# Performance work log

Measured on AMD Instinct MI355X. Metric: run time of the kernel, lower is better.

Reference implementation:

```python
import jax, jax.numpy as jnp
import numpy as np

INF = 1.0e7   # matches torch INF = 1.0 * 10000000.0
EOS_ID = 2
FIN_INIT = -1.0e9  # finite stand-in for torch's -inf init of fin_log_probs


def setup_inputs() -> dict:
    key = jax.random.key(0)
    k1, k2, k3, k4, k5, k6 = jax.random.split(key, 6)
    P, D, S, V = 32, 8, 2048, 128000
    # next-token probability distribution per (prompt, draft)
    logits = jax.random.normal(k1, (P * D, V), dtype=jnp.float32)
    probs = jax.nn.softmax(logits, axis=-1)
    alive_seq = jax.random.randint(k2, (P, D, S), 0, V, dtype=jnp.int32)
    fin_seq = jax.random.randint(k3, (P, D, S), 0, V, dtype=jnp.int32)
    alive_log_probs = -5.0 * jax.random.uniform(k4, (P, D), dtype=jnp.float32)
    fin_log_probs = jnp.full((P, D), FIN_INIT, dtype=jnp.float32)
    still_prompt = jax.random.randint(k5, (P,), 0, 2) == 1
    is_first = jax.random.randint(k6, (P,), 0, 2) == 1
    return {"probs": probs, "alive_seq": alive_seq, "fin_seq": fin_seq,
            "alive_log_probs": alive_log_probs, "fin_log_probs": fin_log_probs,
            "still_prompt": still_prompt, "is_first": is_first, "cur_pos": 1024}


def reference(probs, alive_seq, fin_seq, alive_log_probs, fin_log_probs,
              still_prompt, is_first, cur_pos):
    P, D = alive_log_probs.shape
    V = probs.shape[-1]
    # log-prob accumulation (smoothing=None path)
    log_probs = jnp.log(probs.reshape(P, D, V))                  # (P, D, V)
    curr = alive_log_probs[:, :, None] + log_probs               # (P, D, V)
    # joint topk over beams*vocab
    flat = curr.reshape(P, D * V)
    topk_lp, topk_i = jax.lax.top_k(flat, 2 * D)                 # (P, 2D)
    topk_beam_id = topk_i // V
    topk_tok = topk_i % V
    # first-generation override: only beam 0 counts
    f_vals, f_idx = jax.lax.top_k(log_probs[:, 0, :], 2 * D)     # (P, 2D)
    m = is_first[:, None]
    topk_tok = jnp.where(m, f_idx, topk_tok)
    topk_lp = jnp.where(m, alive_log_probs[:, 0:1] + f_vals, topk_lp)
    # gather parent sequences, write new token at cur_pos
    topk_seq = jnp.take_along_axis(alive_seq, topk_beam_id[:, :, None], axis=1)
    topk_seq = topk_seq.at[:, :, cur_pos].set(topk_tok)
    topk_finished = topk_tok == EOS_ID
    # grow_alive: keep best unfinished
    alive_masked = topk_lp + topk_finished * (-INF)
    na_lp, na_idx = jax.lax.top_k(alive_masked, D)               # (P, D)
    na_seq = jnp.take_along_axis(topk_seq, na_idx[:, :, None], axis=1)
    attention_change_ids = jnp.take_along_axis(topk_beam_id, na_idx, axis=1)
    # grow_fin: keep best finished among old + new
    fin_masked = topk_lp + (~topk_finished) * (-INF)
    cat_seq = jnp.concatenate([fin_seq, topk_seq], axis=1)       # (P, 3D, S)
    cat_lp = jnp.concatenate([fin_log_probs, fin_masked], axis=1)
    nf_lp, nf_idx = jax.lax.top_k(cat_lp, D)
    nf_seq = jnp.take_along_axis(cat_seq, nf_idx[:, :, None], axis=1)
    # still-prompt masking: keep old state, identity attention ids
    sp = still_prompt
    attention_change_ids = jnp.where(sp[:, None], jnp.arange(D), attention_change_ids)
    new_alive_seq = jnp.where(sp[:, None, None], alive_seq, na_seq)
    new_alive_lp = jnp.where(sp[:, None], alive_log_probs, na_lp)
    new_fin_seq = jnp.where(sp[:, None, None], fin_seq, nf_seq)
    new_fin_lp = jnp.where(sp[:, None], fin_log_probs, nf_lp)
    return (attention_change_ids, new_alive_seq, new_alive_lp, new_fin_seq, new_fin_lp)
```

## Files before the change

kernel.cpp:

```cpp
#include <hip/hip_runtime.h>
#include <stdint.h>

#define NEG_BIG -3.0e38f
#define INF_ 10000000.0f
#define EOS_ID 2
#define V_DIM 128000
#define S_DIM 2048
#define CAP 2048

__device__ __forceinline__ bool better(float v1, int i1, float v2, int i2) {
    return (v1 > v2) || (v1 == v2 && i1 < i2);
}
__device__ __forceinline__ float bf16_up(uint16_t u) {
    return __uint_as_float(((uint32_t)u) << 16);
}

__device__ __forceinline__ void hist_b16(uint4 q, int etop, unsigned long long& c0) {
    uint32_t wd[4] = {q.x, q.y, q.z, q.w};
    #pragma unroll
    for (int c = 0; c < 4; ++c) {
        int e0 = (int)((wd[c] >> 7) & 0xFF);
        int e1 = (int)(wd[c] >> 23);
        int k0 = etop - e0; k0 = k0 < 0 ? 0 : (k0 > 7 ? 7 : k0);
        int k1 = etop - e1; k1 = k1 < 0 ? 0 : (k1 > 7 ? 7 : k1);
        c0 += 1ull << (k0 << 3);
        c0 += 1ull << (k1 << 3);
    }
}
__device__ __forceinline__ void hist_f32(float4 q, int etop, unsigned long long& c0) {
    uint32_t u[4] = {__float_as_uint(q.x), __float_as_uint(q.y),
                     __float_as_uint(q.z), __float_as_uint(q.w)};
    #pragma unroll
    for (int c = 0; c < 4; ++c) {
        int e = (int)(u[c] >> 23);
        int k = etop - e; k = k < 0 ? 0 : (k > 7 ? 7 : k);
        c0 += 1ull << (k << 3);
    }
}

__global__ __launch_bounds__(1024) void rowtopk_kernel(const void* probs,
    const uint32_t* finlp, float* ws_val, int* ws_idx) {
    const int r = blockIdx.x;
    const int t = threadIdx.x;
    const int wave = t >> 6, lane = t & 63;
    const bool isbf16 = (finlp[0] == 0xCE6ECE6Eu);

    __shared__ int s_etop, s_B, s_ncand;
    __shared__ uint32_t s_part[16][4];
    __shared__ uint32_t s_bins[8];
    __shared__ uint32_t s_cv[CAP];
    __shared__ int s_ci[CAP];

    const uint4* rowb = (const uint4*)((const uint16_t*)probs + (size_t)r * V_DIM);
    const float4* rowf = (const float4*)((const float*)probs + (size_t)r * V_DIM);
    const int nvec_b = V_DIM / 8;
    const int nvec_f = V_DIM / 4;

    if (t < 64) {
        uint32_t m = 0;
        if (isbf16) {
            uint4 q = rowb[t];
            uint32_t wd[4] = {q.x, q.y, q.z, q.w};
            #pragma unroll
            for (int c = 0; c < 4; ++c) {
                uint32_t lo = wd[c] << 16;
                uint32_t hi = wd[c] & 0xFFFF0000u;
                m = lo > m ? lo : m;
                m = hi > m ? hi : m;
            }
        } else {
            float4 q = rowf[t];
            uint32_t a = __float_as_uint(q.x), b = __float_as_uint(q.y);
            uint32_t c = __float_as_uint(q.z), d = __float_as_uint(q.w);
            m = a > m ? a : m; m = b > m ? b : m;
            m = c > m ? c : m; m = d > m ? d : m;
        }
        #pragma unroll
        for (int s = 1; s < 64; s <<= 1) {
            uint32_t o = (uint32_t)__shfl_xor((int)m, s, 64);
            m = o > m ? o : m;
        }
        if (t == 0) {
            int ea = (int)((m >> 23) & 0xFF);
            s_etop = ea + 3 > 254 ? 254 : ea + 3;
        }
    }
    __syncthreads();

    for (int attempt = 0; attempt < 6; ++attempt) {
        if (t < 64) ((uint32_t*)s_part)[t] = 0;
        if (t == 0) s_B = -1;
        __syncthreads();
        const int etop = s_etop;
        unsigned long long c0 = 0;
        if (isbf16) {
            #pragma unroll
            for (int j = 0; j < 2; ++j) {
                uint4 q0 = rowb[t + 8192 * j];
                uint4 q1 = rowb[t + 8192 * j + 2048];
                uint4 q2 = rowb[t + 8192 * j + 4096];
                uint4 q3 = rowb[t + 8192 * j + 6144];
                hist_b16(q0, etop, c0); hist_b16(q1, etop, c0);
                hist_b16(q2, etop, c0); hist_b16(q3, etop, c0);
            }
        } else {
            #pragma unroll
            for (int j = 0; j < 4; ++j) {
                float4 q0 = rowf[t + 8192 * j];
                float4 q1 = rowf[t + 8192 * j + 2048];
                float4 q2 = rowf[t + 8192 * j + 4096];
                float4 q3 = rowf[t + 8192 * j + 6144];
                hist_f32(q0, etop, c0); hist_f32(q1, etop, c0);
                hist_f32(q2, etop, c0); hist_f32(q3, etop, c0);
            }
        }
        uint32_t f0 = (uint32_t)(c0 & 0xFF)         | (((uint32_t)(c0 >> 8)  & 0xFF) << 16);
        uint32_t f1 = ((uint32_t)(c0 >> 16) & 0xFF) | (((uint32_t)(c0 >> 24) & 0xFF) << 16);
        uint32_t f2 = ((uint32_t)(c0 >> 32) & 0xFF) | (((uint32_t)(c0 >> 40) & 0xFF) << 16);
        uint32_t f3 = ((uint32_t)(c0 >> 48) & 0xFF) | (((uint32_t)(c0 >> 56) & 0xFF) << 16);
        #pragma unroll
        for (int s = 1; s < 64; s <<= 1) {
            f0 += (uint32_t)__shfl_xor((int)f0, s, 64);
            f1 += (uint32_t)__shfl_xor((int)f1, s, 64);
            f2 += (uint32_t)__shfl_xor((int)f2, s, 64);
            f3 += (uint32_t)__shfl_xor((int)f3, s, 64);
        }
        if (lane == 0) {
            s_part[wave][0] = f0; s_part[wave][1] = f1;
            s_part[wave][2] = f2; s_part[wave][3] = f3;
        }
        __syncthreads();
        if (t < 8) {
            uint32_t s = 0;
            for (int w = 0; w < 16; ++w)
                s += (s_part[w][t >> 1] >> ((t & 1) * 16)) & 0xFFFFu;
            s_bins[t] = s;
        }
        __syncthreads();
        if (t == 0) {
            uint32_t cum = 0; int B = -1;
            for (int b = 0; b < 7; ++b) {
                cum += s_bins[b];
                if (cum >= 16) { B = b; break; }
            }
            if (B >= 0) s_B = B; else s_etop = etop - 7;
        }
        __syncthreads();
        if (s_B >= 0) break;
    }

    if (t == 0) s_ncand = 0;
    __syncthreads();
    int ethr = s_etop - s_B; if (ethr < 0) ethr = 0;
    const uint32_t thr = (uint32_t)ethr << 23;

    if (isbf16) {
        #define FILT_B(qv, basepos)                                             \
        {   uint32_t wd[4] = {(qv).x, (qv).y, (qv).z, (qv).w};                  \
            _Pragma("unroll")                                                   \
            for (int c = 0; c < 4; ++c) {                                       \
                uint32_t lo = wd[c] << 16;                                      \
                uint32_t hi = wd[c] & 0xFFFF0000u;                              \
                if (lo >= thr) {                                                \
                    int slot = atomicAdd(&s_ncand, 1);                          \
                    if (slot < CAP) { s_cv[slot] = lo; s_ci[slot] = (basepos) * 8 + c * 2; } \
                }                                                               \
                if (hi >= thr) {                                                \
                    int slot = atomicAdd(&s_ncand, 1);                          \
                    if (slot < CAP) { s_cv[slot] = hi; s_ci[slot] = (basepos) * 8 + c * 2 + 1; } \
                }                                                               \
            }                                                                   \
        }
        for (int base = 0; base < 12288; base += 4096) {
            uint4 q0 = rowb[base + t];
            uint4 q1 = rowb[base + t + 1024];
            uint4 q2 = rowb[base + t + 2048];
            uint4 q3 = rowb[base + t + 3072];
            FILT_B(q0, base + t); FILT_B(q1, base + t + 1024);
            FILT_B(q2, base + t + 2048); FILT_B(q3, base + t + 3072);
        }
        for (int pos = 12288 + t; pos < nvec_b; pos += 1024) {
            uint4 q = rowb[pos];
            FILT_B(q, pos);
        }
    } else {
        #define FILT_F(qv, basepos)                                             \
        {   uint32_t u[4] = {__float_as_uint((qv).x), __float_as_uint((qv).y),  \
                             __float_as_uint((qv).z), __float_as_uint((qv).w)}; \
            _Pragma("unroll")                                                   \
            for (int c = 0; c < 4; ++c) {                                       \
                if (u[c] >= thr) {                                              \
                    int slot = atomicAdd(&s_ncand, 1);                          \
                    if (slot < CAP) { s_cv[slot] = u[c]; s_ci[slot] = (basepos) * 4 + c; } \
                }                                                               \
            }                                                                   \
        }
        for (int base = 0; base < 28672; base += 4096) {
            float4 q0 = rowf[base + t];
            float4 q1 = rowf[base + t + 1024];
            float4 q2 = rowf[base + t + 2048];
            float4 q3 = rowf[base + t + 3072];
            FILT_F(q0, base + t); FILT_F(q1, base + t + 1024);
            FILT_F(q2, base + t + 2048); FILT_F(q3, base + t + 3072);
        }
        for (int pos = 28672 + t; pos < nvec_f; pos += 1024) {
            float4 q = rowf[pos];
            FILT_F(q, pos);
        }
    }
    __syncthreads();
    const int C = s_ncand < CAP ? s_ncand : CAP;

    if (t < 64) {
        uint32_t taken = 0;
        for (int k = 0; k < 16; ++k) {
            float bv = NEG_BIG; int bi = 0x7fffffff; int bs = -1;
            int q = 0;
            for (int j = lane; j < C; j += 64, ++q) {
                if ((taken >> q) & 1u) continue;
                float v = __uint_as_float(s_cv[j]);
                int ix = s_ci[j];
                if (better(v, ix, bv, bi)) { bv = v; bi = ix; bs = j; }
            }
            #pragma unroll
            for (int m = 1; m < 64; m <<= 1) {
                float ov = __shfl_xor(bv, m, 64);
                int oi = __shfl_xor(bi, m, 64);
                int os = __shfl_xor(bs, m, 64);
                if (better(ov, oi, bv, bi)) { bv = ov; bi = oi; bs = os; }
            }
            if (bs >= 0 && (bs & 63) == lane) taken |= 1u << (bs >> 6);
            if (lane == 0) { ws_val[r * 16 + k] = bv; ws_idx[r * 16 + k] = bi; }
        }
    }
}

__global__ __launch_bounds__(256) void selcopy_kernel(
    const void* alive_lp_p, const void* fin_lp_p,
    const int* alive_seq, const int* fin_seq,
    const uint32_t* spw, const uint32_t* isfw, const int* cur_pos_p,
    const float* ws_val, const int* ws_idx, float* out) {
    const int bi = blockIdx.x;
    const int arr = bi >> 8;
    const int rk = bi & 255;
    const int p = rk >> 3, kk = rk & 7;
    const int t = threadIdx.x;
    const int lane = t & 63;

    __shared__ float cv[128]; __shared__ int cflat[128];
    __shared__ float s_alive_lp[8]; __shared__ float s_fin_lp[8];
    __shared__ float topk_lp[16]; __shared__ int topk_tok[16]; __shared__ int topk_beam[16];
    __shared__ int na_sel[8]; __shared__ float na_val[8];
    __shared__ int nf_sel[8]; __shared__ float nf_val[8];
    __shared__ int s_src, s_patch;

    const bool isbf16 = (((const uint32_t*)fin_lp_p)[0] == 0xCE6ECE6Eu);
    uint32_t w1 = (lane < 8) ? spw[lane] : 0u;
    uint32_t w2 = (lane < 8) ? isfw[lane] : 0u;
    const bool bbyte = (__ballot(w1 > 1u || w2 > 1u) != 0ull);

    const bool sp  = bbyte ? (((const uint8_t*)spw)[p] != 0) : (spw[p] != 0u);
    const bool isf = bbyte ? (((const uint8_t*)isfw)[p] != 0) : (isfw[p] != 0u);

    if (t < 8) {
        float a, f;
        if (isbf16) {
            a = bf16_up(((const uint16_t*)alive_lp_p)[p * 8 + t]);
            f = bf16_up(((const uint16_t*)fin_lp_p)[p * 8 + t]);
        } else {
            a = ((const float*)alive_lp_p)[p * 8 + t];
            f = ((const float*)fin_lp_p)[p * 8 + t];
        }
        s_alive_lp[t] = a; s_fin_lp[t] = f;
    }
    __syncthreads();

    if (t < 128) {
        int d = t >> 4, m = t & 15;
        int r = p * 8 + d;
        cv[t] = s_alive_lp[d] + logf(ws_val[r * 16 + m]);
        cflat[t] = d * V_DIM + ws_idx[r * 16 + m];
    }
    __syncthreads();

    if (t < 64) {
        bool taken0 = false, taken1 = false;
        for (int k = 0; k < 16; ++k) {
            float v0 = taken0 ? NEG_BIG : cv[lane];
            int   f0 = taken0 ? 0x7fffffff : cflat[lane];
            float v1 = taken1 ? NEG_BIG : cv[lane + 64];
            int   f1 = taken1 ? 0x7fffffff : cflat[lane + 64];
            float bv; int bf, bj;
            if (better(v0, f0, v1, f1)) { bv = v0; bf = f0; bj = lane; }
            else                        { bv = v1; bf = f1; bj = lane + 64; }
            #pragma unroll
            for (int m = 1; m < 64; m <<= 1) {
                float ov = __shfl_xor(bv, m, 64);
                int   of = __shfl_xor(bf, m, 64);
                int   oj = __shfl_xor(bj, m, 64);
                if (better(ov, of, bv, bf)) { bv = ov; bf = of; bj = oj; }
            }
            if (bj == lane)      taken0 = true;
            if (bj == lane + 64) taken1 = true;
            if (lane == 0) {
                topk_lp[k]   = bv;
                topk_beam[k] = bf / V_DIM;
                topk_tok[k]  = bf % V_DIM;
            }
        }
    }
    __syncthreads();

    if (isf && t < 16) {
        int r0 = p * 8;
        topk_tok[t] = ws_idx[r0 * 16 + t];
        topk_lp[t]  = s_alive_lp[0] + logf(ws_val[r0 * 16 + t]);
    }
    __syncthreads();

    if (t < 64) {
        {
            float mv = NEG_BIG; int mi = 0x7fffffff;
            if (lane < 16) {
                mv = topk_lp[lane] + ((topk_tok[lane] == EOS_ID) ? -INF_ : 0.0f);
                mi = lane;
            }
            bool taken = false;
            for (int k = 0; k < 8; ++k) {
                float bv = taken ? NEG_BIG : mv;
                int   bix = taken ? 0x7fffffff : mi;
                #pragma unroll
                for (int m = 1; m < 64; m <<= 1) {
                    float ov = __shfl_xor(bv, m, 64);
                    int   oi = __shfl_xor(bix, m, 64);
                    if (better(ov, oi, bv, bix)) { bv = ov; bix = oi; }
                }
                if (lane < 16 && bix == mi) taken = true;
                if (lane == 0) { na_sel[k] = bix; na_val[k] = bv; }
            }
        }
        {
            float fv = NEG_BIG; int fi = 0x7fffffff;
            if (lane < 8) { fv = s_fin_lp[lane]; fi = lane; }
            else if (lane < 24) {
                int j = lane - 8;
                fv = topk_lp[j] + ((topk_tok[j] == EOS_ID) ? 0.0f : -INF_);
                fi = lane;
            }
            bool taken = false;
            for (int k = 0; k < 8; ++k) {
                float bv = taken ? NEG_BIG : fv;
                int   bix = taken ? 0x7fffffff : fi;
                #pragma unroll
                for (int m = 1; m < 64; m <<= 1) {
                    float ov = __shfl_xor(bv, m, 64);
                    int   oi = __shfl_xor(bix, m, 64);
                    if (better(ov, oi, bv, bix)) { bv = ov; bix = oi; }
                }
                if (lane < 24 && bix == fi) taken = true;
                if (lane == 0) { nf_sel[k] = bix; nf_val[k] = bv; }
            }
        }
    }
    __syncthreads();

    float* out_attn = out;
    float* out_alp  = out + 256 + 524288;
    float* out_flp  = out + 512 + 2 * 524288;
    if (t == 0) {
        int na = na_sel[kk], nf = nf_sel[kk];
        if (arr == 0) {
            out_attn[p * 8 + kk] = (float)(sp ? kk : topk_beam[na]);
            out_alp[p * 8 + kk]  = sp ? s_alive_lp[kk] : na_val[kk];
            out_flp[p * 8 + kk]  = sp ? s_fin_lp[kk]   : nf_val[kk];
        }
        int src, patch;
        if (arr == 0) {
            if (sp) { src = p * 8 + kk; patch = -1; }
            else    { src = p * 8 + topk_beam[na]; patch = topk_tok[na]; }
        } else {
            if (sp) { src = (p * 8 + kk) | (1 << 30); patch = -1; }
            else if (nf < 8) { src = (p * 8 + nf) | (1 << 30); patch = -1; }
            else { int j = nf - 8; src = p * 8 + topk_beam[j]; patch = topk_tok[j]; }
        }
        s_src = src; s_patch = patch;
    }
    __syncthreads();

    const int src = s_src, patch = s_patch;
    const int* s = ((src >> 30) & 1) ? fin_seq : alive_seq;
    const int4* srow = (const int4*)(s + (size_t)(src & 0x3FFFFFFF) * S_DIM);
    float* drow = out + (arr ? (512 + 524288) : 256) + (size_t)rk * S_DIM;
    const int cp = cur_pos_p[0];

    for (int i = t; i < S_DIM / 4; i += 256) {
        int4 v = srow[i];
        if (patch >= 0) {
            int s0 = i * 4;
            if (s0 + 0 == cp) v.x = patch;
            if (s0 + 1 == cp) v.y = patch;
            if (s0 + 2 == cp) v.z = patch;
            if (s0 + 3 == cp) v.w = patch;
        }
        ((float4*)drow)[i] = make_float4((float)v.x, (float)v.y, (float)v.z, (float)v.w);
    }
}

extern "C" void kernel_launch(void* const* d_in, const int* in_sizes, int n_in,
                              void* d_out, int out_size, void* d_ws, size_t ws_size,
                              hipStream_t stream) {
    (void)in_sizes; (void)n_in; (void)out_size; (void)ws_size;
    const void* probs      = d_in[0];
    const int*  alive_seq  = (const int*)d_in[1];
    const int*  fin_seq    = (const int*)d_in[2];
    const void* alive_lp   = d_in[3];
    const void* fin_lp     = d_in[4];
    const uint32_t* spw    = (const uint32_t*)d_in[5];
    const uint32_t* isfw   = (const uint32_t*)d_in[6];
    const int*  cur_pos    = (const int*)d_in[7];

    float* ws_val = (float*)d_ws;
    int*   ws_idx = (int*)((char*)d_ws + 16384);

    rowtopk_kernel<<<256, 1024, 0, stream>>>(probs, (const uint32_t*)fin_lp, ws_val, ws_idx);
    selcopy_kernel<<<512, 256, 0, stream>>>(alive_lp, fin_lp, alive_seq, fin_seq,
                                            spw, isfw, cur_pos, ws_val, ws_idx,
                                            (float*)d_out);
}
```

Baseline: 236.1 us.

## Reuse register-held row sample for threshold histogram and filter pass

Each thread now loads a fixed quarter-row sample into registers once. It takes the max over that sample, instead of over only the first 64 vectors, and builds the exponent histogram from those registers rather than re-reading the whole row on every attempt. The filter pass reuses the held registers and loads only the remaining chunks, so each row is read from global memory roughly once instead of twice or more. The candidate buffer grows from 2048 to 6144 entries to absorb the larger candidate counts a sample-based threshold can produce, at the cost of more LDS and register pressure.

New measurement: 255.1 us. +8.0%, slower.

```diff
diff --git a/kernel.cpp b/kernel.cpp
--- a/kernel.cpp
+++ b/kernel.cpp
@@ -6,7 +6,7 @@
 #define EOS_ID 2
 #define V_DIM 128000
 #define S_DIM 2048
-#define CAP 2048
+#define CAP 6144
 
 __device__ __forceinline__ bool better(float v1, int i1, float v2, int i2) {
     return (v1 > v2) || (v1 == v2 && i1 < i2);
@@ -27,9 +27,8 @@
         c0 += 1ull << (k1 << 3);
     }
 }
-__device__ __forceinline__ void hist_f32(float4 q, int etop, unsigned long long& c0) {
-    uint32_t u[4] = {__float_as_uint(q.x), __float_as_uint(q.y),
-                     __float_as_uint(q.z), __float_as_uint(q.w)};
+__device__ __forceinline__ void hist_f32u(uint4 q, int etop, unsigned long long& c0) {
+    uint32_t u[4] = {q.x, q.y, q.z, q.w};
     #pragma unroll
     for (int c = 0; c < 4; ++c) {
         int e = (int)(u[c] >> 23);
@@ -48,42 +47,52 @@
     __shared__ int s_etop, s_B, s_ncand;
     __shared__ uint32_t s_part[16][4];
     __shared__ uint32_t s_bins[8];
+    __shared__ uint32_t s_wmax[16];
     __shared__ uint32_t s_cv[CAP];
     __shared__ int s_ci[CAP];
 
     const uint4* rowb = (const uint4*)((const uint16_t*)probs + (size_t)r * V_DIM);
-    const float4* rowf = (const float4*)((const float*)probs + (size_t)r * V_DIM);
-    const int nvec_b = V_DIM / 8;
-    const int nvec_f = V_DIM / 4;
-
-    if (t < 64) {
-        uint32_t m = 0;
-        if (isbf16) {
-            uint4 q = rowb[t];
-            uint32_t wd[4] = {q.x, q.y, q.z, q.w};
-            #pragma unroll
-            for (int c = 0; c < 4; ++c) {
-                uint32_t lo = wd[c] << 16;
-                uint32_t hi = wd[c] & 0xFFFF0000u;
-                m = lo > m ? lo : m;
-                m = hi > m ? hi : m;
-            }
-        } else {
-            float4 q = rowf[t];
-            uint32_t a = __float_as_uint(q.x), b = __float_as_uint(q.y);
-            uint32_t c = __float_as_uint(q.z), d = __float_as_uint(q.w);
-            m = a > m ? a : m; m = b > m ? b : m;
-            m = c > m ? c : m; m = d > m ? d : m;
-        }
-        #pragma unroll
-        for (int s = 1; s < 64; s <<= 1) {
-            uint32_t o = (uint32_t)__shfl_xor((int)m, s, 64);
-            m = o > m ? o : m;
-        }
-        if (t == 0) {
-            int ea = (int)((m >> 23) & 0xFF);
-            s_etop = ea + 3 > 254 ? 254 : ea + 3;
-        }
+    const uint4* rowu = (const uint4*)((const float*)probs + (size_t)r * V_DIM);
+
+    uint4 q0, q1, q2, q3, q4, q5, q6, q7;
+    if (isbf16) {
+        q0 = rowb[t];          q1 = rowb[4096 + t];
+        q2 = rowb[8192 + t];   q3 = rowb[12288 + t];
+    } else {
+        q0 = rowu[t];          q1 = rowu[4096 + t];
+        q2 = rowu[8192 + t];   q3 = rowu[12288 + t];
+        q4 = rowu[16384 + t];  q5 = rowu[20480 + t];
+        q6 = rowu[24576 + t];  q7 = rowu[28672 + t];
+    }
+
+    uint32_t m = 0;
+    if (isbf16) {
+        #define MB(q) { uint32_t w[4]={(q).x,(q).y,(q).z,(q).w};                 \
+            _Pragma("unroll")                                                    \
+            for (int c = 0; c < 4; ++c) {                                        \
+                uint32_t lo = w[c] << 16, hi = w[c] & 0xFFFF0000u;               \
+                m = lo > m ? lo : m; m = hi > m ? hi : m; } }
+        MB(q0) MB(q1) MB(q2) MB(q3)
+        #undef MB
+    } else {
+        #define MF(q) { uint32_t w[4]={(q).x,(q).y,(q).z,(q).w};                 \
+            _Pragma("unroll")                                                    \
+            for (int c = 0; c < 4; ++c) { m = w[c] > m ? w[c] : m; } }
+        MF(q0) MF(q1) MF(q2) MF(q3) MF(q4) MF(q5) MF(q6) MF(q7)
+        #undef MF
+    }
+    #pragma unroll
+    for (int s = 1; s < 64; s <<= 1) {
+        uint32_t o = (uint32_t)__shfl_xor((int)m, s, 64);
+        m = o > m ? o : m;
+    }
+    if (lane == 0) s_wmax[wave] = m;
+    __syncthreads();
+    if (t == 0) {
+        uint32_t mm = 0;
+        for (int w = 0; w < 16; ++w) mm = s_wmax[w] > mm ? s_wmax[w] : mm;
+        int ea = (int)(mm >> 23);
+        s_etop = ea + 1 > 254 ? 254 : ea + 1;
     }
     __syncthreads();
 
@@ -94,25 +103,13 @@
         const int etop = s_etop;
         unsigned long long c0 = 0;
         if (isbf16) {
-            #pragma unroll
-            for (int j = 0; j < 2; ++j) {
-                uint4 q0 = rowb[t + 8192 * j];
-                uint4 q1 = rowb[t + 8192 * j + 2048];
-                uint4 q2 = rowb[t + 8192 * j + 4096];
-                uint4 q3 = rowb[t + 8192 * j + 6144];
-                hist_b16(q0, etop, c0); hist_b16(q1, etop, c0);
-                hist_b16(q2, etop, c0); hist_b16(q3, etop, c0);
-            }
+            hist_b16(q0, etop, c0); hist_b16(q1, etop, c0);
+            hist_b16(q2, etop, c0); hist_b16(q3, etop, c0);
         } else {
-            #pragma unroll
-            for (int j = 0; j < 4; ++j) {
-                float4 q0 = rowf[t + 8192 * j];
-                float4 q1 = rowf[t + 8192 * j + 2048];
-                float4 q2 = rowf[t + 8192 * j + 4096];
-                float4 q3 = rowf[t + 8192 * j + 6144];
-                hist_f32(q0, etop, c0); hist_f32(q1, etop, c0);
-                hist_f32(q2, etop, c0); hist_f32(q3, etop, c0);
-            }
+            hist_f32u(q0, etop, c0); hist_f32u(q1, etop, c0);
+            hist_f32u(q2, etop, c0); hist_f32u(q3, etop, c0);
+            hist_f32u(q4, etop, c0); hist_f32u(q5, etop, c0);
+            hist_f32u(q6, etop, c0); hist_f32u(q7, etop, c0);
         }
         uint32_t f0 = (uint32_t)(c0 & 0xFF)         | (((uint32_t)(c0 >> 8)  & 0xFF) << 16);
         uint32_t f1 = ((uint32_t)(c0 >> 16) & 0xFF) | (((uint32_t)(c0 >> 24) & 0xFF) << 16);
@@ -151,61 +148,78 @@
 
     if (t == 0) s_ncand = 0;
     __syncthreads();
-    int ethr = s_etop - s_B; if (ethr < 0) ethr = 0;
+    const int Bsel = (s_B >= 0) ? s_B : 6;
+    int ethr = s_etop - Bsel; if (ethr < 0) ethr = 0;
     const uint32_t thr = (uint32_t)ethr << 23;
 
+    #define FILT_B(qv, basepos)                                                 \
+    {   uint32_t wd[4] = {(qv).x, (qv).y, (qv).z, (qv).w};                      \
+        _Pragma("unroll")                                                       \
+        for (int c = 0; c < 4; ++c) {                                           \
+            uint32_t lo = wd[c] << 16;                                          \
+            uint32_t hi = wd[c] & 0xFFFF0000u;                                  \
+            if (lo >= thr) {                                                    \
+                int slot = atomicAdd(&s_ncand, 1);                              \
+                if (slot < CAP) { s_cv[slot] = lo; s_ci[slot] = (basepos) * 8 + c * 2; } \
+            }                                                                   \
+            if (hi >= thr) {                                                    \
+                int slot = atomicAdd(&s_ncand, 1);                              \
+                if (slot < CAP) { s_cv[slot] = hi; s_ci[slot] = (basepos) * 8 + c * 2 + 1; } \
+            }                                                                   \
+        }                                                                       \
+    }
+    #define FILT_FU(qv, basepos)                                                \
+    {   uint32_t u[4] = {(qv).x, (qv).y, (qv).z, (qv).w};                       \
+        _Pragma("unroll")                                                       \
+        for (int c = 0; c < 4; ++c) {                                           \
+            if (u[c] >= thr) {                                                  \
+                int slot = atomicAdd(&s_ncand, 1);                              \
+                if (slot < CAP) { s_cv[slot] = u[c]; s_ci[slot] = (basepos) * 4 + c; } \
+            }                                                                   \
+        }                                                                       \
+    }
+
     if (isbf16) {
-        #define FILT_B(qv, basepos)                                             \
-        {   uint32_t wd[4] = {(qv).x, (qv).y, (qv).z, (qv).w};                  \
-            _Pragma("unroll")                                                   \
-            for (int c = 0; c < 4; ++c) {                                       \
-                uint32_t lo = wd[c] << 16;                                      \
-                uint32_t hi = wd[c] & 0xFFFF0000u;                              \
-                if (lo >= thr) {                                                \
-                    int slot = atomicAdd(&s_ncand, 1);                          \
-                    if (slot < CAP) { s_cv[slot] = lo; s_ci[slot] = (basepos) * 8 + c * 2; } \
-                }                                                               \
-                if (hi >= thr) {                                                \
-                    int slot = atomicAdd(&s_ncand, 1);                          \
-                    if (slot < CAP) { s_cv[slot] = hi; s_ci[slot] = (basepos) * 8 + c * 2 + 1; } \
-                }                                                               \
-            }                                                                   \
-        }
-        for (int base = 0; base < 12288; base += 4096) {
-            uint4 q0 = rowb[base + t];
-            uint4 q1 = rowb[base + t + 1024];
-            uint4 q2 = rowb[base + t + 2048];
-            uint4 q3 = rowb[base + t + 3072];
-            FILT_B(q0, base + t); FILT_B(q1, base + t + 1024);
-            FILT_B(q2, base + t + 2048); FILT_B(q3, base + t + 3072);
-        }
-        for (int pos = 12288 + t; pos < nvec_b; pos += 1024) {
-            uint4 q = rowb[pos];
-            FILT_B(q, pos);
+        FILT_B(q0, t); FILT_B(q1, 4096 + t);
+        FILT_B(q2, 8192 + t); FILT_B(q3, 12288 + t);
+        #pragma unroll
+        for (int g = 0; g < 3; ++g) {
+            const int base = g * 4096;
+            uint4 a0 = rowb[base + 1024 + t];
+            uint4 a1 = rowb[base + 2048 + t];
+            uint4 a2 = rowb[base + 3072 + t];
+            FILT_B(a0, base + 1024 + t);
+            FILT_B(a1, base + 2048 + t);
+            FILT_B(a2, base + 3072 + t);
+        }
+        {
+            uint4 a0 = rowb[13312 + t];
+            uint4 a1 = rowb[14336 + t];
+            FILT_B(a0, 13312 + t);
+            FILT_B(a1, 14336 + t);
+            if (t < 640) { uint4 a2 = rowb[15360 + t]; FILT_B(a2, 15360 + t); }
         }
     } else {
-        #define FILT_F(qv, basepos)                                             \
-        {   uint32_t u[4] = {__float_as_uint((qv).x), __float_as_uint((qv).y),  \
-                             __float_as_uint((qv).z), __float_as_uint((qv).w)}; \
-            _Pragma("unroll")                                                   \
-            for (int c = 0; c < 4; ++c) {                                       \
-                if (u[c] >= thr) {                                              \
-                    int slot = atomicAdd(&s_ncand, 1);                          \
-                    if (slot < CAP) { s_cv[slot] = u[c]; s_ci[slot] = (basepos) * 4 + c; } \
-                }                                                               \
-            }                                                                   \
-        }
-        for (int base = 0; base < 28672; base += 4096) {
-            float4 q0 = rowf[base + t];
-            float4 q1 = rowf[base + t + 1024];
-            float4 q2 = rowf[base + t + 2048];
-            float4 q3 = rowf[base + t + 3072];
-            FILT_F(q0, base + t); FILT_F(q1, base + t + 1024);
-            FILT_F(q2, base + t + 2048); FILT_F(q3, base + t + 3072);
-        }
-        for (int pos = 28672 + t; pos < nvec_f; pos += 1024) {
-            float4 q = rowf[pos];
-            FILT_F(q, pos);
+        FILT_FU(q0, t);           FILT_FU(q1, 4096 + t);
+        FILT_FU(q2, 8192 + t);    FILT_FU(q3, 12288 + t);
+        FILT_FU(q4, 16384 + t);   FILT_FU(q5, 20480 + t);
+        FILT_FU(q6, 24576 + t);   FILT_FU(q7, 28672 + t);
+        #pragma unroll
+        for (int g = 0; g < 7; ++g) {
+            const int base = g * 4096;
+            uint4 a0 = rowu[base + 1024 + t];
+            uint4 a1 = rowu[base + 2048 + t];
+            uint4 a2 = rowu[base + 3072 + t];
+            FILT_FU(a0, base + 1024 + t);
+            FILT_FU(a1, base + 2048 + t);
+            FILT_FU(a2, base + 3072 + t);
+        }
+        {
+            uint4 a0 = rowu[29696 + t];
+            uint4 a1 = rowu[30720 + t];
+            FILT_FU(a0, 29696 + t);
+            FILT_FU(a1, 30720 + t);
+            if (t < 256) { uint4 a2 = rowu[31744 + t]; FILT_FU(a2, 31744 + t); }
         }
     }
     __syncthreads();
@@ -223,10 +237,10 @@
                 if (better(v, ix, bv, bi)) { bv = v; bi = ix; bs = j; }
             }
             #pragma unroll
-            for (int m = 1; m < 64; m <<= 1) {
-                float ov = __shfl_xor(bv, m, 64);
-                int oi = __shfl_xor(bi, m, 64);
-                int os = __shfl_xor(bs, m, 64);
+            for (int mm = 1; mm < 64; mm <<= 1) {
+                float ov = __shfl_xor(bv, mm, 64);
+                int oi = __shfl_xor(bi, mm, 64);
+                int os = __shfl_xor(bs, mm, 64);
                 if (better(ov, oi, bv, bi)) { bv = ov; bi = oi; bs = os; }
             }
             if (bs >= 0 && (bs & 63) == lane) taken |= 1u << (bs >> 6);
```
